# Performance work log

Hardware: AMD Instinct MI355X
Metric: run time of the kernel (lower is better)

## Reference

```python
import jax, jax.numpy as jnp
import numpy as np

N_NODES = 100000
N_EDGES = 1600000
IN_CH = 128
HID = 128
N_GRAPHS = 512


def setup_inputs() -> dict:
    key = jax.random.key(0)
    ks = jax.random.split(key, 16)
    x = jax.random.normal(ks[0], (N_NODES, IN_CH), dtype=jnp.float32)
    edge_index = jax.random.randint(ks[1], (2, N_EDGES), 0, N_NODES, dtype=jnp.int64)
    batch = jnp.sort(jax.random.randint(ks[2], (N_NODES,), 0, N_GRAPHS, dtype=jnp.int64))
    s = 1.0 / np.sqrt(HID)
    params = {
        'W1': jax.random.normal(ks[3], (IN_CH, HID), jnp.float32) / np.sqrt(IN_CH),
        'b1': jnp.zeros((HID,), jnp.float32),
        'W2': jax.random.normal(ks[4], (HID, HID), jnp.float32) * s,
        'b2': jnp.zeros((HID,), jnp.float32),
        'W3': jax.random.normal(ks[5], (HID, HID), jnp.float32) * s,
        'b3': jnp.zeros((HID,), jnp.float32),
        'Wf1': jax.random.normal(ks[6], (2 * HID, HID), jnp.float32) / np.sqrt(2 * HID),
        'bf1': jnp.zeros((HID,), jnp.float32),
        'Wf2': jax.random.normal(ks[7], (HID, HID // 2), jnp.float32) * s,
        'bf2': jnp.zeros((HID // 2,), jnp.float32),
        'Wf3': jax.random.normal(ks[8], (HID // 2, 1), jnp.float32) / np.sqrt(HID // 2),
        'bf3': jnp.zeros((1,), jnp.float32),
    }
    return {'x': x, 'edge_index': edge_index, 'batch': batch, 'n_graphs': N_GRAPHS, **params}


def _gcn_norm(edge_index, n_nodes):
    # add self-loops, then symmetric normalization D^{-1/2} (A+I) D^{-1/2}
    loops = jnp.arange(n_nodes, dtype=edge_index.dtype)
    src = jnp.concatenate([edge_index[0], loops])
    dst = jnp.concatenate([edge_index[1], loops])
    deg = jax.ops.segment_sum(jnp.ones_like(dst, dtype=jnp.float32), dst, num_segments=n_nodes)
    dinv = jnp.where(deg > 0, jax.lax.rsqrt(deg), 0.0)
    norm = dinv[src] * dinv[dst]  # [E + N]
    return src, dst, norm


def _gcn_conv(h, W, b, src, dst, norm, n_nodes):
    h = h @ W                                   # [N, H]
    msg = h[src] * norm[:, None]                # gather + edge scale
    agg = jax.ops.segment_sum(msg, dst, num_segments=n_nodes)  # scatter-add
    return agg + b


def reference(x, edge_index, batch, n_graphs, W1, b1, W2, b2, W3, b3, Wf1, bf1, Wf2, bf2, Wf3, bf3):
    n_nodes = x.shape[0]
    src, dst, norm = _gcn_norm(edge_index, n_nodes)

    h = jax.nn.relu(_gcn_conv(x, W1, b1, src, dst, norm, n_nodes))
    h_res = h
    h = jax.nn.relu(_gcn_conv(h, W2, b2, src, dst, norm, n_nodes)) + h_res
    h_res = h
    h = jax.nn.relu(_gcn_conv(h, W3, b3, src, dst, norm, n_nodes)) + h_res

    ones = jnp.ones((n_nodes, 1), jnp.float32)
    counts = jax.ops.segment_sum(ones, batch, num_segments=n_graphs)  # [G,1]
    g_mean = jax.ops.segment_sum(h, batch, num_segments=n_graphs) / jnp.maximum(counts, 1.0)
    g_max = jax.ops.segment_max(h, batch, num_segments=n_graphs)
    g = jnp.concatenate([g_mean, g_max], axis=1)  # [G, 2H]

    # MLP head (dropout is identity at inference)
    g = jax.nn.relu(g @ Wf1 + bf1)
    g = jax.nn.relu(g @ Wf2 + bf2)
    return g @ Wf3 + bf3  # [G, 1]
```

## Files before the change

### kernel.cpp

```cpp
#include <hip/hip_runtime.h>
#include <hip/hip_bf16.h>

#define NBMAX 256
#define BSH 9
#define BMSK 511
#define CHUNK 4096
#define CAPB 10240
#define WPREPB 192

typedef __attribute__((ext_vector_type(8))) short short8;
typedef __attribute__((ext_vector_type(4))) float f32x4;

__device__ inline unsigned short bf16_rne(float x) {
    unsigned u = __float_as_uint(x);
    u = (u + 0x7FFFu + ((u >> 16) & 1u)) >> 16;
    return (unsigned short)u;
}
__device__ inline float bf16_to_f(unsigned short h) {
    return __uint_as_float(((unsigned)h) << 16);
}
__device__ inline void split2(float v, short& h, short& lo) {
    unsigned short hb = bf16_rne(v);
    h = (short)hb;
    lo = (short)bf16_rne(v - bf16_to_f(hb));
}


__global__ __launch_bounds__(256) void k_pre(const int* __restrict__ src,
                                             const int* __restrict__ dst, int E, int NB,
                                             int* __restrict__ bcur,
                                             unsigned* __restrict__ pairs,
                                             const float* __restrict__ W1,
                                             const float* __restrict__ W2,
                                             const float* __restrict__ W3,
                                             unsigned short* __restrict__ WH,
                                             unsigned short* __restrict__ WL) {
    __shared__ int lcnt[NBMAX];
    __shared__ int loff[NBMAX];
    __shared__ int gbase[NBMAX];
    __shared__ unsigned plds[CHUNK];
    __shared__ unsigned char blds[CHUNK];
    int t = threadIdx.x;

    if (blockIdx.x < WPREPB) {
        int wi = blockIdx.x >> 6;
        int idx = (blockIdx.x & 63) * 256 + t;
        const float* W = (wi == 0) ? W1 : (wi == 1) ? W2 : W3;
        int j = idx & 7;
        int lane = (idx >> 3) & 63;
        int ct = (idx >> 9) & 7;
        int kc = idx >> 12;
        int k = kc * 32 + (lane >> 4) * 8 + j;
        int col = ct * 16 + (lane & 15);
        float v = W[k * 128 + col];
        unsigned short hb = bf16_rne(v);
        WH[wi * 16384 + idx] = hb;
        WL[wi * 16384 + idx] = bf16_rne(v - bf16_to_f(hb));
        return;
    }

    int base = (blockIdx.x - WPREPB) * CHUNK;
    for (int i = t; i < NBMAX; i += 256) lcnt[i] = 0;
    __syncthreads();
    int rank[16], bid[16];
    unsigned pk[16];
#pragma unroll
    for (int i = 0; i < 16; i++) {
        int e = base + i * 256 + t;
        if (e < E) {
            int d = dst[e];
            int b = d >> BSH;
            bid[i] = b;
            pk[i] = ((unsigned)(d & BMSK) << 17) | (unsigned)src[e];
            rank[i] = atomicAdd(&lcnt[b], 1);
        } else bid[i] = -1;
    }
    __syncthreads();
    loff[t] = lcnt[t];
    __syncthreads();
    for (int off = 1; off < NBMAX; off <<= 1) {
        int x = (t >= off) ? loff[t - off] : 0;
        __syncthreads();
        loff[t] += x;
        __syncthreads();
    }
    if (t < NB) {
        int c = lcnt[t];
        gbase[t] = c ? atomicAdd(&bcur[t], c) : 0;
    }
    __syncthreads();
#pragma unroll
    for (int i = 0; i < 16; i++) {
        int b = bid[i];
        if (b >= 0) {
            int pos = loff[b] - lcnt[b] + rank[i];
            plds[pos] = pk[i];
            blds[pos] = (unsigned char)b;
        }
    }
    __syncthreads();
    int total = min(E - base, CHUNK);
    for (int i = t; i < total; i += 256) {
        int b = blds[i];
        int local = gbase[b] + (i - (loff[b] - lcnt[b]));
        if (local < CAPB) pairs[b * CAPB + local] = plds[i];
    }
}

__global__ __launch_bounds__(512) void k_node(const unsigned* __restrict__ pairs,
                                              const int* __restrict__ bcur, int N,
                                              int2* __restrict__ row,
                                              float* __restrict__ dinv,
                                              int* __restrict__ csr_src) {
    __shared__ int cnt_l[512];
    __shared__ int cur_l[512];
    __shared__ int wsum[8];
    __shared__ unsigned plds[CAPB];
    __shared__ int stage[CAPB];
    int t = threadIdx.x;
    int lane = t & 63, wv = t >> 6;
    int b = blockIdx.x;
    int n0 = b << BSH;
    int nn = min(512, N - n0);
    cnt_l[t] = 0;
    __syncthreads();
    int e0 = b * CAPB;
    int len = min(bcur[b], CAPB);
    for (int i = t; i < len; i += 512) {
        unsigned p = pairs[e0 + i];
        plds[i] = p;
        atomicAdd(&cnt_l[p >> 17], 1);
    }
    __syncthreads();
    int c = cnt_l[t];
    int v = c;
#pragma unroll
    for (int off = 1; off < 64; off <<= 1) {
        int x = __shfl_up(v, off);
        if (lane >= off) v += x;
    }
    if (lane == 63) wsum[wv] = v;
    __syncthreads();
    if (t < 8) {
        int wval = wsum[t];
#pragma unroll
        for (int off = 1; off < 8; off <<= 1) {
            int x = __shfl_up(wval, off);
            if (lane >= off) wval += x;
        }
        wsum[t] = wval;
    }
    __syncthreads();
    int prefix = (wv > 0) ? wsum[wv - 1] : 0;
    int lstart = prefix + v - c;
    if (t < nn) {
        row[n0 + t] = make_int2(e0 + lstart, e0 + lstart + c);
        dinv[n0 + t] = rsqrtf((float)c + 1.0f);
    }
    cur_l[t] = lstart;
    __syncthreads();
    for (int i = t; i < len; i += 512) {
        unsigned p = plds[i];
        int r = atomicAdd(&cur_l[p >> 17], 1);
        stage[r] = (int)(p & 0x1FFFFu);
    }
    __syncthreads();
    for (int i = t; i < len; i += 512) csr_src[e0 + i] = stage[i];
}


__global__ __launch_bounds__(256) void k_gemm3f(const float* __restrict__ A,
                                                const unsigned short* __restrict__ WH,
                                                const unsigned short* __restrict__ WL,
                                                const float* __restrict__ dinv,
                                                unsigned short* __restrict__ U, int N) {
    __shared__ unsigned short sW[32768];
    {
        int t = threadIdx.x;
#pragma unroll
        for (int i = 0; i < 8; i++) {
            __builtin_amdgcn_global_load_lds(
                (const __attribute__((address_space(1))) void*)(WH + t * 8 + i * 2048),
                (__attribute__((address_space(3))) void*)(sW + t * 8 + i * 2048), 16, 0, 0);
        }
#pragma unroll
        for (int i = 0; i < 8; i++) {
            __builtin_amdgcn_global_load_lds(
                (const __attribute__((address_space(1))) void*)(WL + t * 8 + i * 2048),
                (__attribute__((address_space(3))) void*)(sW + 16384 + t * 8 + i * 2048), 16, 0, 0);
        }
    }
    __syncthreads();

    int wv = threadIdx.x >> 6;
    int l = threadIdx.x & 63;
    int quad = l >> 4;
    int lm = l & 15;
    int rowBase = blockIdx.x * 128 + wv * 32;

    f32x4 acc[2][8] = {};

    int r0 = rowBase + lm;
    int r1 = rowBase + 16 + lm;

#pragma unroll
    for (int kc = 0; kc < 4; kc++) {
        int k0 = kc * 32 + quad * 8;
        short8 ah0, al0, ah1, al1;
        float av0[8] = {}, av1[8] = {};
        if (r0 < N) {
            float4 a = *(const float4*)&A[(size_t)r0 * 128 + k0];
            float4 b = *(const float4*)&A[(size_t)r0 * 128 + k0 + 4];
            av0[0] = a.x; av0[1] = a.y; av0[2] = a.z; av0[3] = a.w;
            av0[4] = b.x; av0[5] = b.y; av0[6] = b.z; av0[7] = b.w;
        }
        if (r1 < N) {
            float4 a = *(const float4*)&A[(size_t)r1 * 128 + k0];
            float4 b = *(const float4*)&A[(size_t)r1 * 128 + k0 + 4];
            av1[0] = a.x; av1[1] = a.y; av1[2] = a.z; av1[3] = a.w;
            av1[4] = b.x; av1[5] = b.y; av1[6] = b.z; av1[7] = b.w;
        }
#pragma unroll
        for (int j = 0; j < 8; j++) {
            short h, lo;
            split2(av0[j], h, lo); ah0[j] = h; al0[j] = lo;
            split2(av1[j], h, lo); ah1[j] = h; al1[j] = lo;
        }
#pragma unroll
        for (int ct = 0; ct < 8; ct++) {
            int fo = ((kc * 8 + ct) * 64 + l) * 8;
            short8 wh = *(const short8*)&sW[fo];
            short8 wl = *(const short8*)&sW[16384 + fo];
            acc[0][ct] = __builtin_amdgcn_mfma_f32_16x16x32_bf16(ah0, wh, acc[0][ct], 0, 0, 0);
            acc[0][ct] = __builtin_amdgcn_mfma_f32_16x16x32_bf16(ah0, wl, acc[0][ct], 0, 0, 0);
            acc[0][ct] = __builtin_amdgcn_mfma_f32_16x16x32_bf16(al0, wh, acc[0][ct], 0, 0, 0);
            acc[1][ct] = __builtin_amdgcn_mfma_f32_16x16x32_bf16(ah1, wh, acc[1][ct], 0, 0, 0);
            acc[1][ct] = __builtin_amdgcn_mfma_f32_16x16x32_bf16(ah1, wl, acc[1][ct], 0, 0, 0);
            acc[1][ct] = __builtin_amdgcn_mfma_f32_16x16x32_bf16(al1, wh, acc[1][ct], 0, 0, 0);
        }
    }

#pragma unroll
    for (int rt = 0; rt < 2; rt++) {
#pragma unroll
        for (int reg = 0; reg < 4; reg++) {
            int row = rowBase + rt * 16 + quad * 4 + reg;
            if (row < N) {
                float dv = dinv[row];
#pragma unroll
                for (int ct = 0; ct < 8; ct++) {
                    U[(size_t)row * 128 + ct * 16 + lm] = bf16_rne(dv * acc[rt][ct][reg]);
                }
            }
        }
    }
}

__global__ __launch_bounds__(512, 4) void k_gemm3s(const unsigned short* __restrict__ AH,
                                                   const unsigned short* __restrict__ AL,
                                                   const unsigned short* __restrict__ WH,
                                                   const unsigned short* __restrict__ WL,
                                                   const float* __restrict__ dinv,
                                                   unsigned short* __restrict__ U, int N) {
    __shared__ unsigned short sW[32768];
    {
        int t = threadIdx.x;
#pragma unroll
        for (int i = 0; i < 4; i++) {
            __builtin_amdgcn_global_load_lds(
                (const __attribute__((address_space(1))) void*)(WH + t * 8 + i * 4096),
                (__attribute__((address_space(3))) void*)(sW + t * 8 + i * 4096), 16, 0, 0);
        }
#pragma unroll
        for (int i = 0; i < 4; i++) {
            __builtin_amdgcn_global_load_lds(
                (const __attribute__((address_space(1))) void*)(WL + t * 8 + i * 4096),
                (__attribute__((address_space(3))) void*)(sW + 16384 + t * 8 + i * 4096), 16, 0, 0);
        }
    }
    __syncthreads();

    int wv = threadIdx.x >> 6;
    int l = threadIdx.x & 63;
    int quad = l >> 4;
    int lm = l & 15;
    int rowBase = blockIdx.x * 256 + wv * 32;

    f32x4 acc[2][8] = {};

    int r0 = rowBase + lm;
    int r1 = rowBase + 16 + lm;

#pragma unroll
    for (int kc = 0; kc < 4; kc++) {
        int k0 = kc * 32 + quad * 8;
        short8 ah0 = {}, al0 = {}, ah1 = {}, al1 = {};
        if (r0 < N) {
            ah0 = *(const short8*)&AH[(size_t)r0 * 128 + k0];
            al0 = *(const short8*)&AL[(size_t)r0 * 128 + k0];
        }
        if (r1 < N) {
            ah1 = *(const short8*)&AH[(size_t)r1 * 128 + k0];
            al1 = *(const short8*)&AL[(size_t)r1 * 128 + k0];
        }
#pragma unroll
        for (int ct = 0; ct < 8; ct++) {
            int fo = ((kc * 8 + ct) * 64 + l) * 8;
            short8 wh = *(const short8*)&sW[fo];
            short8 wl = *(const short8*)&sW[16384 + fo];
            acc[0][ct] = __builtin_amdgcn_mfma_f32_16x16x32_bf16(ah0, wh, acc[0][ct], 0, 0, 0);
            acc[0][ct] = __builtin_amdgcn_mfma_f32_16x16x32_bf16(ah0, wl, acc[0][ct], 0, 0, 0);
            acc[0][ct] = __builtin_amdgcn_mfma_f32_16x16x32_bf16(al0, wh, acc[0][ct], 0, 0, 0);
            acc[1][ct] = __builtin_amdgcn_mfma_f32_16x16x32_bf16(ah1, wh, acc[1][ct], 0, 0, 0);
            acc[1][ct] = __builtin_amdgcn_mfma_f32_16x16x32_bf16(ah1, wl, acc[1][ct], 0, 0, 0);
            acc[1][ct] = __builtin_amdgcn_mfma_f32_16x16x32_bf16(al1, wh, acc[1][ct], 0, 0, 0);
        }
    }

#pragma unroll
    for (int rt = 0; rt < 2; rt++) {
#pragma unroll
        for (int reg = 0; reg < 4; reg++) {
            int row = rowBase + rt * 16 + quad * 4 + reg;
            if (row < N) {
                float dv = dinv[row];
#pragma unroll
                for (int ct = 0; ct < 8; ct++) {
                    U[(size_t)row * 128 + ct * 16 + lm] = bf16_rne(dv * acc[rt][ct][reg]);
                }
            }
        }
    }
}


template <int RES>
__global__ __launch_bounds__(256) void k_agg(const unsigned short* __restrict__ U,
                                             const int2* __restrict__ row,
                                             const int* __restrict__ csr_src,
                                             const float* __restrict__ dinv,
                                             const float* __restrict__ bias,
                                             unsigned short* __restrict__ HH,
                                             unsigned short* __restrict__ HL, int N) {
    int wave = threadIdx.x >> 6;
    int lane = threadIdx.x & 63;
    int n = blockIdx.x * 4 + wave;
    if (n >= N) return;
    int grp = lane >> 4;
    int li = lane & 15;
    int2 rw = row[n];
    int e0 = rw.x, e1 = rw.y;
    int len = e1 - e0;
    int q0 = e0 + ((len * grp) >> 2);
    int q1 = e0 + ((len * (grp + 1)) >> 2);

    float a0 = 0.f, a1 = 0.f, a2 = 0.f, a3 = 0.f;
    float a4 = 0.f, a5 = 0.f, a6 = 0.f, a7 = 0.f;
    float b0 = 0.f, b1 = 0.f, b2 = 0.f, b3 = 0.f;
    float b4 = 0.f, b5 = 0.f, b6 = 0.f, b7 = 0.f;

    int e = q0;
    for (; e + 4 <= q1; e += 4) {
        int s0 = csr_src[e];
        int s1 = csr_src[e + 1];
        int s2 = csr_src[e + 2];
        int s3 = csr_src[e + 3];
        uint4 r0 = *(const uint4*)&U[(size_t)s0 * 128 + li * 8];
        uint4 r1 = *(const uint4*)&U[(size_t)s1 * 128 + li * 8];
        uint4 r2 = *(const uint4*)&U[(size_t)s2 * 128 + li * 8];
        uint4 r3 = *(const uint4*)&U[(size_t)s3 * 128 + li * 8];
        a0 += __uint_as_float(r0.x << 16);        a1 += __uint_as_float(r0.x & 0xFFFF0000u);
        a2 += __uint_as_float(r0.y << 16);        a3 += __uint_as_float(r0.y & 0xFFFF0000u);
        a4 += __uint_as_float(r0.z << 16);        a5 += __uint_as_float(r0.z & 0xFFFF0000u);
        a6 += __uint_as_float(r0.w << 16);        a7 += __uint_as_float(r0.w & 0xFFFF0000u);
        b0 += __uint_as_float(r1.x << 16);        b1 += __uint_as_float(r1.x & 0xFFFF0000u);
        b2 += __uint_as_float(r1.y << 16);        b3 += __uint_as_float(r1.y & 0xFFFF0000u);
        b4 += __uint_as_float(r1.z << 16);        b5 += __uint_as_float(r1.z & 0xFFFF0000u);
        b6 += __uint_as_float(r1.w << 16);        b7 += __uint_as_float(r1.w & 0xFFFF0000u);
        a0 += __uint_as_float(r2.x << 16);        a1 += __uint_as_float(r2.x & 0xFFFF0000u);
        a2 += __uint_as_float(r2.y << 16);        a3 += __uint_as_float(r2.y & 0xFFFF0000u);
        a4 += __uint_as_float(r2.z << 16);        a5 += __uint_as_float(r2.z & 0xFFFF0000u);
        a6 += __uint_as_float(r2.w << 16);        a7 += __uint_as_float(r2.w & 0xFFFF0000u);
        b0 += __uint_as_float(r3.x << 16);        b1 += __uint_as_float(r3.x & 0xFFFF0000u);
        b2 += __uint_as_float(r3.y << 16);        b3 += __uint_as_float(r3.y & 0xFFFF0000u);
        b4 += __uint_as_float(r3.z << 16);        b5 += __uint_as_float(r3.z & 0xFFFF0000u);
        b6 += __uint_as_float(r3.w << 16);        b7 += __uint_as_float(r3.w & 0xFFFF0000u);
    }
    if (e + 2 <= q1) {
        int s0 = csr_src[e];
        int s1 = csr_src[e + 1];
        uint4 r0 = *(const uint4*)&U[(size_t)s0 * 128 + li * 8];
        uint4 r1 = *(const uint4*)&U[(size_t)s1 * 128 + li * 8];
        a0 += __uint_as_float(r0.x << 16);        a1 += __uint_as_float(r0.x & 0xFFFF0000u);
        a2 += __uint_as_float(r0.y << 16);        a3 += __uint_as_float(r0.y & 0xFFFF0000u);
        a4 += __uint_as_float(r0.z << 16);        a5 += __uint_as_float(r0.z & 0xFFFF0000u);
        a6 += __uint_as_float(r0.w << 16);        a7 += __uint_as_float(r0.w & 0xFFFF0000u);
        b0 += __uint_as_float(r1.x << 16);        b1 += __uint_as_float(r1.x & 0xFFFF0000u);
        b2 += __uint_as_float(r1.y << 16);        b3 += __uint_as_float(r1.y & 0xFFFF0000u);
        b4 += __uint_as_float(r1.z << 16);        b5 += __uint_as_float(r1.z & 0xFFFF0000u);
        b6 += __uint_as_float(r1.w << 16);        b7 += __uint_as_float(r1.w & 0xFFFF0000u);
        e += 2;
    }
    if (e < q1) {
        int s0 = csr_src[e];
        uint4 r0 = *(const uint4*)&U[(size_t)s0 * 128 + li * 8];
        a0 += __uint_as_float(r0.x << 16);        a1 += __uint_as_float(r0.x & 0xFFFF0000u);
        a2 += __uint_as_float(r0.y << 16);        a3 += __uint_as_float(r0.y & 0xFFFF0000u);
        a4 += __uint_as_float(r0.z << 16);        a5 += __uint_as_float(r0.z & 0xFFFF0000u);
        a6 += __uint_as_float(r0.w << 16);        a7 += __uint_as_float(r0.w & 0xFFFF0000u);
    }
    a0 += b0; a1 += b1; a2 += b2; a3 += b3;
    a4 += b4; a5 += b5; a6 += b6; a7 += b7;

    a0 += __shfl_xor(a0, 16); a1 += __shfl_xor(a1, 16);
    a2 += __shfl_xor(a2, 16); a3 += __shfl_xor(a3, 16);
    a4 += __shfl_xor(a4, 16); a5 += __shfl_xor(a5, 16);
    a6 += __shfl_xor(a6, 16); a7 += __shfl_xor(a7, 16);
    a0 += __shfl_xor(a0, 32); a1 += __shfl_xor(a1, 32);
    a2 += __shfl_xor(a2, 32); a3 += __shfl_xor(a3, 32);
    a4 += __shfl_xor(a4, 32); a5 += __shfl_xor(a5, 32);
    a6 += __shfl_xor(a6, 32); a7 += __shfl_xor(a7, 32);

    if (grp == 0) {
        uint4 qs = *(const uint4*)&U[(size_t)n * 128 + li * 8];
        float4 bi0 = *(const float4*)&bias[li * 8];
        float4 bi1 = *(const float4*)&bias[li * 8 + 4];
        float dn = dinv[n];
        float v0 = fmaxf(dn * (a0 + __uint_as_float(qs.x << 16)) + bi0.x, 0.f);
        float v1 = fmaxf(dn * (a1 + __uint_as_float(qs.x & 0xFFFF0000u)) + bi0.y, 0.f);
        float v2 = fmaxf(dn * (a2 + __uint_as_float(qs.y << 16)) + bi0.z, 0.f);
        float v3 = fmaxf(dn * (a3 + __uint_as_float(qs.y & 0xFFFF0000u)) + bi0.w, 0.f);
        float v4 = fmaxf(dn * (a4 + __uint_as_float(qs.z << 16)) + bi1.x, 0.f);
        float v5 = fmaxf(dn * (a5 + __uint_as_float(qs.z & 0xFFFF0000u)) + bi1.y, 0.f);
        float v6 = fmaxf(dn * (a6 + __uint_as_float(qs.w << 16)) + bi1.z, 0.f);
        float v7 = fmaxf(dn * (a7 + __uint_as_float(qs.w & 0xFFFF0000u)) + bi1.w, 0.f);
        size_t hi = (size_t)n * 128 + li * 8;
        if (RES) {
            uint4 rh = *(const uint4*)&HH[hi];
            uint4 rl = *(const uint4*)&HL[hi];
            v0 += __uint_as_float(rh.x << 16) + __uint_as_float(rl.x << 16);
            v1 += __uint_as_float(rh.x & 0xFFFF0000u) + __uint_as_float(rl.x & 0xFFFF0000u);
            v2 += __uint_as_float(rh.y << 16) + __uint_as_float(rl.y << 16);
            v3 += __uint_as_float(rh.y & 0xFFFF0000u) + __uint_as_float(rl.y & 0xFFFF0000u);
            v4 += __uint_as_float(rh.z << 16) + __uint_as_float(rl.z << 16);
            v5 += __uint_as_float(rh.z & 0xFFFF0000u) + __uint_as_float(rl.z & 0xFFFF0000u);
            v6 += __uint_as_float(rh.w << 16) + __uint_as_float(rl.w << 16);
            v7 += __uint_as_float(rh.w & 0xFFFF0000u) + __uint_as_float(rl.w & 0xFFFF0000u);
        }
        float vv[8] = {v0, v1, v2, v3, v4, v5, v6, v7};
        unsigned hw[4], lw[4];
#pragma unroll
        for (int j = 0; j < 4; j++) {
            unsigned short h0 = bf16_rne(vv[2 * j]);
            unsigned short h1 = bf16_rne(vv[2 * j + 1]);
            unsigned short l0 = bf16_rne(vv[2 * j] - bf16_to_f(h0));
            unsigned short l1 = bf16_rne(vv[2 * j + 1] - bf16_to_f(h1));
            hw[j] = (unsigned)h0 | ((unsigned)h1 << 16);
            lw[j] = (unsigned)l0 | ((unsigned)l1 << 16);
        }
        *(uint4*)&HH[hi] = make_uint4(hw[0], hw[1], hw[2], hw[3]);
        *(uint4*)&HL[hi] = make_uint4(lw[0], lw[1], lw[2], lw[3]);
    }
}


__global__ __launch_bounds__(512) void k_head(const unsigned short* __restrict__ HH,
                                              const unsigned short* __restrict__ HL,
                                              const int* __restrict__ batch, int N, int G,
                                              const float* __restrict__ Wf1,
                                              const float* __restrict__ bf1,
                                              const float* __restrict__ Wf2,
                                              const float* __restrict__ bf2,
                                              const float* __restrict__ Wf3,
                                              const float* __restrict__ bf3,
                                              float* __restrict__ out) {
    __shared__ float ssum0[512];
    __shared__ float ssum1[512];
    __shared__ float smax0[512];
    __shared__ float smax1[512];
    __shared__ float grow[256];
    __shared__ float o1[128];
    __shared__ float o2[64];
    int g = blockIdx.x;
    int t = threadIdx.x;
    int i0, i1;
    {
        int lo = 0, hi = N;
        while (lo < hi) { int m = (lo + hi) >> 1; if (batch[m] < g) lo = m + 1; else hi = m; }
        i0 = lo;
        lo = i0; hi = N;
        while (lo < hi) { int m = (lo + hi) >> 1; if (batch[m] < g + 1) lo = m + 1; else hi = m; }
        i1 = lo;
    }
    int cp = t & 63;
    int sl = t >> 6;
    int cn = i1 - i0;
    int a0 = i0 + ((cn * sl) >> 3);
    int a1 = i0 + ((cn * (sl + 1)) >> 3);
    float s0 = 0.f, s1 = 0.f, m0 = -3.4e38f, m1 = -3.4e38f;
    for (int i = a0; i < a1; i++) {
        size_t idx = (size_t)i * 128 + cp * 2;
        unsigned hh = *(const unsigned*)&HH[idx];
        unsigned hl = *(const unsigned*)&HL[idx];
        float vlo = __uint_as_float(hh << 16) + __uint_as_float(hl << 16);
        float vhi = __uint_as_float(hh & 0xFFFF0000u) + __uint_as_float(hl & 0xFFFF0000u);
        s0 += vlo; m0 = fmaxf(m0, vlo);
        s1 += vhi; m1 = fmaxf(m1, vhi);
    }
    ssum0[t] = s0; ssum1[t] = s1;
    smax0[t] = m0; smax1[t] = m1;
    __syncthreads();
    if (t < 64) {
        float st0 = 0.f, st1 = 0.f, mt0 = -3.4e38f, mt1 = -3.4e38f;
#pragma unroll
        for (int k = 0; k < 8; k++) {
            st0 += ssum0[t + 64 * k]; st1 += ssum1[t + 64 * k];
            mt0 = fmaxf(mt0, smax0[t + 64 * k]); mt1 = fmaxf(mt1, smax1[t + 64 * k]);
        }
        grow[2 * t]       = (cn > 0) ? st0 / (float)cn : 0.f;
        grow[2 * t + 1]   = (cn > 0) ? st1 / (float)cn : 0.f;
        grow[128 + 2 * t]     = (cn > 0) ? mt0 : 0.f;
        grow[128 + 2 * t + 1] = (cn > 0) ? mt1 : 0.f;
    }
    __syncthreads();
    if (t < 128) {
        float acc = bf1[t];
#pragma unroll 8
        for (int k = 0; k < 256; k++) acc = fmaf(grow[k], Wf1[k * 128 + t], acc);
        o1[t] = fmaxf(acc, 0.f);
    }
    __syncthreads();
    if (t < 64) {
        float a2 = bf2[t];
#pragma unroll 8
        for (int k = 0; k < 128; k++) a2 = fmaf(o1[k], Wf2[k * 64 + t], a2);
        o2[t] = fmaxf(a2, 0.f);
    }
    __syncthreads();
    if (t < 64) {
        float p = o2[t] * Wf3[t];
        for (int off = 32; off > 0; off >>= 1) p += __shfl_down(p, off);
        if (t == 0) out[g] = p + bf3[0];
    }
}


extern "C" void kernel_launch(void* const* d_in, const int* in_sizes, int n_in,
                              void* d_out, int out_size, void* d_ws, size_t ws_size,
                              hipStream_t stream) {
    const float* x = (const float*)d_in[0];
    const int* ei = (const int*)d_in[1];
    const int* batch = (const int*)d_in[2];
    const float* W1 = (const float*)d_in[4];
    const float* b1 = (const float*)d_in[5];
    const float* W2 = (const float*)d_in[6];
    const float* b2 = (const float*)d_in[7];
    const float* W3 = (const float*)d_in[8];
    const float* b3 = (const float*)d_in[9];
    const float* Wf1 = (const float*)d_in[10];
    const float* bf1 = (const float*)d_in[11];
    const float* Wf2 = (const float*)d_in[12];
    const float* bf2 = (const float*)d_in[13];
    const float* Wf3 = (const float*)d_in[14];
    const float* bf3 = (const float*)d_in[15];

    const int N = in_sizes[0] / 128;
    const int E = in_sizes[1] / 2;
    const int G = out_size;

    const int* src = ei;
    const int* dst = ei + E;

    char* w = (char*)d_ws;
    size_t off = 0;
    auto alloc = [&](size_t bytes) -> void* {
        void* p = w + off;
        off += (bytes + 255) / 256 * 256;
        return p;
    };
    const int NB = (N + BMSK) >> BSH;
    unsigned short* U = (unsigned short*)alloc((size_t)N * 128 * 2);
    unsigned short* HHp = (unsigned short*)alloc((size_t)N * 128 * 2);
    unsigned short* HLp = (unsigned short*)alloc((size_t)N * 128 * 2);
    unsigned* pairs = (unsigned*)alloc((size_t)NB * CAPB * 4);
    int* csr_src = (int*)alloc((size_t)NB * CAPB * 4);
    int2* row = (int2*)alloc((size_t)N * 8);
    float* dinv = (float*)alloc((size_t)N * 4);
    int* bcur = (int*)alloc(NBMAX * 4);
    unsigned short* WH = (unsigned short*)alloc(3 * 16384 * 2);
    unsigned short* WL = (unsigned short*)alloc(3 * 16384 * 2);
    float* out = (float*)d_out;

    const int ebk = (E + CHUNK - 1) / CHUNK;

    hipMemsetAsync(bcur, 0, NBMAX * sizeof(int), stream);

    k_pre<<<dim3(WPREPB + ebk), dim3(256), 0, stream>>>(src, dst, E, NB, bcur, pairs,
                                                        W1, W2, W3, WH, WL);
    k_node<<<dim3(NB), dim3(512), 0, stream>>>(pairs, bcur, N, row, dinv, csr_src);

    const int gemmGridF = (N + 127) / 128;
    const int gemmGridS = (N + 255) / 256;
    const int aggGrid = (N + 3) / 4;

    k_gemm3f<<<dim3(gemmGridF), dim3(256), 0, stream>>>(x, WH, WL, dinv, U, N);
    k_agg<0><<<dim3(aggGrid), dim3(256), 0, stream>>>(U, row, csr_src, dinv, b1, HHp, HLp, N);
    k_gemm3s<<<dim3(gemmGridS), dim3(512), 0, stream>>>(HHp, HLp, WH + 16384, WL + 16384, dinv, U, N);
    k_agg<1><<<dim3(aggGrid), dim3(256), 0, stream>>>(U, row, csr_src, dinv, b2, HHp, HLp, N);
    k_gemm3s<<<dim3(gemmGridS), dim3(512), 0, stream>>>(HHp, HLp, WH + 32768, WL + 32768, dinv, U, N);
    k_agg<1><<<dim3(aggGrid), dim3(256), 0, stream>>>(U, row, csr_src, dinv, b3, HHp, HLp, N);

    k_head<<<dim3(G), dim3(512), 0, stream>>>(HHp, HLp, batch, N, G, Wf1, bf1, Wf2, bf2, Wf3, bf3, out);
}
```

Baseline: 443.5 us.

## Split CSR build blocks into node halves and loop two tiles per first-GEMM block

k_node now launches two blocks per node bucket. Each block handles 256 destination nodes and re-reads the bucket's pairs from global memory instead of caching them in LDS. Shared memory drops to a smaller staging buffer, with a direct global-scatter fallback when a half overflows it. The first GEMM now processes two 128-row tiles per block so the LDS weight load is amortised over more rows. The trade-off is extra global reads of pairs and fewer GEMM blocks, in exchange for more k_node parallelism and occupancy.

```diff
diff --git a/kernel.cpp b/kernel.cpp
--- a/kernel.cpp
+++ b/kernel.cpp
@@ -7,6 +7,7 @@
 #define CHUNK 4096
 #define CAPB 10240
 #define WPREPB 192
+#define SHCAP 6144
 
 typedef __attribute__((ext_vector_type(8))) short short8;
 typedef __attribute__((ext_vector_type(4))) float f32x4;
@@ -112,60 +113,91 @@
                                               int2* __restrict__ row,
                                               float* __restrict__ dinv,
                                               int* __restrict__ csr_src) {
-    __shared__ int cnt_l[512];
-    __shared__ int cur_l[512];
-    __shared__ int wsum[8];
-    __shared__ unsigned plds[CAPB];
-    __shared__ int stage[CAPB];
+    __shared__ int cnt_l[256];
+    __shared__ int cur_l[256];
+    __shared__ int wsum[4];
+    __shared__ int h0tot;
+    __shared__ int stage[SHCAP];
     int t = threadIdx.x;
     int lane = t & 63, wv = t >> 6;
-    int b = blockIdx.x;
-    int n0 = b << BSH;
-    int nn = min(512, N - n0);
-    cnt_l[t] = 0;
+    int b = blockIdx.x >> 1;
+    int h = blockIdx.x & 1;
+    int n0 = (b << BSH) + (h << 8);
+    int nn = min(256, N - n0);
+    if (t < 256) cnt_l[t] = 0;
+    if (t == 0) h0tot = 0;
     __syncthreads();
     int e0 = b * CAPB;
     int len = min(bcur[b], CAPB);
+    int c0 = 0;
     for (int i = t; i < len; i += 512) {
         unsigned p = pairs[e0 + i];
-        plds[i] = p;
-        atomicAdd(&cnt_l[p >> 17], 1);
-    }
-    __syncthreads();
-    int c = cnt_l[t];
-    int v = c;
-#pragma unroll
-    for (int off = 1; off < 64; off <<= 1) {
-        int x = __shfl_up(v, off);
-        if (lane >= off) v += x;
-    }
-    if (lane == 63) wsum[wv] = v;
-    __syncthreads();
-    if (t < 8) {
+        int node = (int)(p >> 17);
+        c0 += (node < 256) ? 1 : 0;
+        if ((node >> 8) == h) atomicAdd(&cnt_l[node & 255], 1);
+    }
+#pragma unroll
+    for (int off = 32; off > 0; off >>= 1) c0 += __shfl_down(c0, off);
+    if (lane == 0 && c0) atomicAdd(&h0tot, c0);
+    __syncthreads();
+    int half0 = h0tot;
+    int base0 = e0 + (h ? half0 : 0);
+    int halfLen = h ? (len - half0) : half0;
+    int c = 0, v = 0;
+    if (t < 256) {
+        c = cnt_l[t];
+        v = c;
+#pragma unroll
+        for (int off = 1; off < 64; off <<= 1) {
+            int x = __shfl_up(v, off);
+            if (lane >= off) v += x;
+        }
+        if (lane == 63) wsum[wv] = v;
+    }
+    __syncthreads();
+    if (t < 4) {
         int wval = wsum[t];
 #pragma unroll
-        for (int off = 1; off < 8; off <<= 1) {
+        for (int off = 1; off < 4; off <<= 1) {
             int x = __shfl_up(wval, off);
             if (lane >= off) wval += x;
         }
         wsum[t] = wval;
     }
     __syncthreads();
-    int prefix = (wv > 0) ? wsum[wv - 1] : 0;
-    int lstart = prefix + v - c;
-    if (t < nn) {
-        row[n0 + t] = make_int2(e0 + lstart, e0 + lstart + c);
-        dinv[n0 + t] = rsqrtf((float)c + 1.0f);
-    }
-    cur_l[t] = lstart;
-    __syncthreads();
-    for (int i = t; i < len; i += 512) {
-        unsigned p = plds[i];
-        int r = atomicAdd(&cur_l[p >> 17], 1);
-        stage[r] = (int)(p & 0x1FFFFu);
-    }
-    __syncthreads();
-    for (int i = t; i < len; i += 512) csr_src[e0 + i] = stage[i];
+    if (t < 256) {
+        int prefix = (wv > 0) ? wsum[wv - 1] : 0;
+        int lstart = prefix + v - c;
+        if (t < nn) {
+            row[n0 + t] = make_int2(base0 + lstart, base0 + lstart + c);
+            dinv[n0 + t] = rsqrtf((float)c + 1.0f);
+        }
+        cur_l[t] = lstart;
+    }
+    __syncthreads();
+    if (halfLen <= SHCAP) {
+        for (int i = t; i < len; i += 512) {
+            unsigned p = pairs[e0 + i];
+            int node = (int)(p >> 17);
+            if ((node >> 8) == h) {
+                int r = atomicAdd(&cur_l[node & 255], 1);
+                stage[r] = (int)(p & 0x1FFFFu);
+            }
+        }
+        __syncthreads();
+        for (int i = t; i < halfLen; i += 512) csr_src[base0 + i] = stage[i];
+    } else {
+        if (t < 256) cur_l[t] += base0;
+        __syncthreads();
+        for (int i = t; i < len; i += 512) {
+            unsigned p = pairs[e0 + i];
+            int node = (int)(p >> 17);
+            if ((node >> 8) == h) {
+                int r = atomicAdd(&cur_l[node & 255], 1);
+                csr_src[r] = (int)(p & 0x1FFFFu);
+            }
+        }
+    }
 }
 
 
@@ -196,60 +228,63 @@
     int l = threadIdx.x & 63;
     int quad = l >> 4;
     int lm = l & 15;
-    int rowBase = blockIdx.x * 128 + wv * 32;
-
-    f32x4 acc[2][8] = {};
-
-    int r0 = rowBase + lm;
-    int r1 = rowBase + 16 + lm;
-
-#pragma unroll
-    for (int kc = 0; kc < 4; kc++) {
-        int k0 = kc * 32 + quad * 8;
-        short8 ah0, al0, ah1, al1;
-        float av0[8] = {}, av1[8] = {};
-        if (r0 < N) {
-            float4 a = *(const float4*)&A[(size_t)r0 * 128 + k0];
-            float4 b = *(const float4*)&A[(size_t)r0 * 128 + k0 + 4];
-            av0[0] = a.x; av0[1] = a.y; av0[2] = a.z; av0[3] = a.w;
-            av0[4] = b.x; av0[5] = b.y; av0[6] = b.z; av0[7] = b.w;
-        }
-        if (r1 < N) {
-            float4 a = *(const float4*)&A[(size_t)r1 * 128 + k0];
-            float4 b = *(const float4*)&A[(size_t)r1 * 128 + k0 + 4];
-            av1[0] = a.x; av1[1] = a.y; av1[2] = a.z; av1[3] = a.w;
-            av1[4] = b.x; av1[5] = b.y; av1[6] = b.z; av1[7] = b.w;
-        }
-#pragma unroll
-        for (int j = 0; j < 8; j++) {
-            short h, lo;
-            split2(av0[j], h, lo); ah0[j] = h; al0[j] = lo;
-            split2(av1[j], h, lo); ah1[j] = h; al1[j] = lo;
-        }
-#pragma unroll
-        for (int ct = 0; ct < 8; ct++) {
-            int fo = ((kc * 8 + ct) * 64 + l) * 8;
-            short8 wh = *(const short8*)&sW[fo];
-            short8 wl = *(const short8*)&sW[16384 + fo];
-            acc[0][ct] = __builtin_amdgcn_mfma_f32_16x16x32_bf16(ah0, wh, acc[0][ct], 0, 0, 0);
-            acc[0][ct] = __builtin_amdgcn_mfma_f32_16x16x32_bf16(ah0, wl, acc[0][ct], 0, 0, 0);
-            acc[0][ct] = __builtin_amdgcn_mfma_f32_16x16x32_bf16(al0, wh, acc[0][ct], 0, 0, 0);
-            acc[1][ct] = __builtin_amdgcn_mfma_f32_16x16x32_bf16(ah1, wh, acc[1][ct], 0, 0, 0);
-            acc[1][ct] = __builtin_amdgcn_mfma_f32_16x16x32_bf16(ah1, wl, acc[1][ct], 0, 0, 0);
-            acc[1][ct] = __builtin_amdgcn_mfma_f32_16x16x32_bf16(al1, wh, acc[1][ct], 0, 0, 0);
-        }
-    }
-
-#pragma unroll
-    for (int rt = 0; rt < 2; rt++) {
-#pragma unroll
-        for (int reg = 0; reg < 4; reg++) {
-            int row = rowBase + rt * 16 + quad * 4 + reg;
-            if (row < N) {
-                float dv = dinv[row];
-#pragma unroll
-                for (int ct = 0; ct < 8; ct++) {
-                    U[(size_t)row * 128 + ct * 16 + lm] = bf16_rne(dv * acc[rt][ct][reg]);
+
+    for (int tile = 0; tile < 2; tile++) {
+        int rowBase = (blockIdx.x * 2 + tile) * 128 + wv * 32;
+
+        f32x4 acc[2][8] = {};
+
+        int r0 = rowBase + lm;
+        int r1 = rowBase + 16 + lm;
+
+#pragma unroll
+        for (int kc = 0; kc < 4; kc++) {
+            int k0 = kc * 32 + quad * 8;
+            short8 ah0, al0, ah1, al1;
+            float av0[8] = {}, av1[8] = {};
+            if (r0 < N) {
+                float4 a = *(const float4*)&A[(size_t)r0 * 128 + k0];
+                float4 b = *(const float4*)&A[(size_t)r0 * 128 + k0 + 4];
+                av0[0] = a.x; av0[1] = a.y; av0[2] = a.z; av0[3] = a.w;
+                av0[4] = b.x; av0[5] = b.y; av0[6] = b.z; av0[7] = b.w;
+            }
+            if (r1 < N) {
+                float4 a = *(const float4*)&A[(size_t)r1 * 128 + k0];
+                float4 b = *(const float4*)&A[(size_t)r1 * 128 + k0 + 4];
+                av1[0] = a.x; av1[1] = a.y; av1[2] = a.z; av1[3] = a.w;
+                av1[4] = b.x; av1[5] = b.y; av1[6] = b.z; av1[7] = b.w;
+            }
+#pragma unroll
+            for (int j = 0; j < 8; j++) {
+                short hh, lo;
+                split2(av0[j], hh, lo); ah0[j] = hh; al0[j] = lo;
+                split2(av1[j], hh, lo); ah1[j] = hh; al1[j] = lo;
+            }
+#pragma unroll
+            for (int ct = 0; ct < 8; ct++) {
+                int fo = ((kc * 8 + ct) * 64 + l) * 8;
+                short8 wh = *(const short8*)&sW[fo];
+                short8 wl = *(const short8*)&sW[16384 + fo];
+                acc[0][ct] = __builtin_amdgcn_mfma_f32_16x16x32_bf16(ah0, wh, acc[0][ct], 0, 0, 0);
+                acc[0][ct] = __builtin_amdgcn_mfma_f32_16x16x32_bf16(ah0, wl, acc[0][ct], 0, 0, 0);
+                acc[0][ct] = __builtin_amdgcn_mfma_f32_16x16x32_bf16(al0, wh, acc[0][ct], 0, 0, 0);
+                acc[1][ct] = __builtin_amdgcn_mfma_f32_16x16x32_bf16(ah1, wh, acc[1][ct], 0, 0, 0);
+                acc[1][ct] = __builtin_amdgcn_mfma_f32_16x16x32_bf16(ah1, wl, acc[1][ct], 0, 0, 0);
+                acc[1][ct] = __builtin_amdgcn_mfma_f32_16x16x32_bf16(al1, wh, acc[1][ct], 0, 0, 0);
+            }
+        }
+
+#pragma unroll
+        for (int rt = 0; rt < 2; rt++) {
+#pragma unroll
+            for (int reg = 0; reg < 4; reg++) {
+                int rowi = rowBase + rt * 16 + quad * 4 + reg;
+                if (rowi < N) {
+                    float dv = dinv[rowi];
+#pragma unroll
+                    for (int ct = 0; ct < 8; ct++) {
+                        U[(size_t)rowi * 128 + ct * 16 + lm] = bf16_rne(dv * acc[rt][ct][reg]);
+                    }
                 }
             }
         }
@@ -597,9 +632,9 @@
 
     k_pre<<<dim3(WPREPB + ebk), dim3(256), 0, stream>>>(src, dst, E, NB, bcur, pairs,
                                                         W1, W2, W3, WH, WL);
-    k_node<<<dim3(NB), dim3(512), 0, stream>>>(pairs, bcur, N, row, dinv, csr_src);
-
-    const int gemmGridF = (N + 127) / 128;
+    k_node<<<dim3(NB * 2), dim3(512), 0, stream>>>(pairs, bcur, N, row, dinv, csr_src);
+
+    const int gemmGridF = (N + 255) / 256;
     const int gemmGridS = (N + 255) / 256;
     const int aggGrid = (N + 3) / 4;
 
```

After: 461.6 us. +4.1%, slower.
